# Performance work log

Hardware: AMD Instinct MI355X
Metric: run time of the kernel (lower is better)

The kernel has to match this reference:

```python
import jax, jax.numpy as jnp
import numpy as np

B, H, T, D = 2, 16, 2048, 64


def setup_inputs() -> dict:
    key = jax.random.key(0)
    kq, kk, kv = jax.random.split(key, 3)
    Q = jax.random.normal(kq, (B, H, T, D), dtype=jnp.float32)
    K = jax.random.normal(kk, (B, H, T, D), dtype=jnp.float32)
    V = jax.random.normal(kv, (B, H, T, D), dtype=jnp.float32)
    return {"Q": Q, "K": K, "V": V}


def reference(Q, K, V):
    # Q,K,V: [B,H,T,D]; causal self-attention with 1/sqrt(D) temperature.
    Bq, Hq, Tq, Dq = Q.shape
    temperature = jnp.asarray(Dq, Q.dtype) ** 0.5
    # [B,H,T,T] attention scores
    scores = jnp.einsum('bhqd,bhkd->bhqk', Q, K) / temperature
    causal = jnp.tril(jnp.ones((Tq, Tq), dtype=bool))  # [T,T]
    scores = jnp.where(causal[None, None, :, :], scores, jnp.finfo(Q.dtype).min)
    weights = jax.nn.softmax(scores, axis=-1)
    return jnp.einsum('bhqk,bhkd->bhqd', weights, V)
```

## Files before the change

### kernel.cpp

```cpp
#include <hip/hip_runtime.h>
#include <hip/hip_bf16.h>
#include <math.h>


#define BATCH 2
#define HEADS 16
#define SEQ   2048
#define DIM   64
#define QTILE 64
#define KTILE 64
#define NBH   (BATCH * HEADS)
#define NQT   (SEQ / QTILE)
#define NKT_G (SEQ / KTILE)
#define TILE_SHORTS 4096

typedef __attribute__((ext_vector_type(8))) short bf16x8;
typedef __attribute__((ext_vector_type(4))) short s16x4;
typedef __attribute__((ext_vector_type(2))) unsigned u32x2;
typedef __attribute__((ext_vector_type(4))) float f32x4;

__device__ inline short f2bf(float f) {
    unsigned u = __builtin_bit_cast(unsigned, f);
    u += 0x7fff + ((u >> 16) & 1);
    return (short)(u >> 16);
}

__device__ inline unsigned cvtpk(float a, float b) {
    unsigned r;
    asm("v_cvt_pk_bf16_f32 %0, %1, %2" : "=v"(r) : "v"(a), "v"(b));
    return r;
}

__device__ inline void gload16(const void* g, void* l) {
    __builtin_amdgcn_global_load_lds(
        (const __attribute__((address_space(1))) unsigned*)g,
        (__attribute__((address_space(3))) unsigned*)l, 16, 0, 0);
}

__global__ __launch_bounds__(256)
void prep_kv(const float* __restrict__ K, const float* __restrict__ V,
             short* __restrict__ Kswz, short* __restrict__ Vtswz) {
    const int tile = blockIdx.x;
    const int tid  = threadIdx.x;
    const float* Ksrc = K + (size_t)tile * TILE_SHORTS;
    const float* Vsrc = V + (size_t)tile * TILE_SHORTS;
    char* Kdst = (char*)(Kswz  + (size_t)tile * TILE_SHORTS);
    char* Vdst = (char*)(Vtswz + (size_t)tile * TILE_SHORTS);

    __shared__ float vt[64][65];

    const int r  = tid >> 2;
    const int c0 = (tid & 3) * 16;

    {
        short kh[16];
        #pragma unroll
        for (int j = 0; j < 16; j += 4) {
            const f32x4 v = *reinterpret_cast<const f32x4*>(Ksrc + (size_t)r * 64 + c0 + j);
            kh[j] = f2bf(v[0]); kh[j+1] = f2bf(v[1]); kh[j+2] = f2bf(v[2]); kh[j+3] = f2bf(v[3]);
        }
        const unsigned swz  = ((unsigned)r & 7) << 4;
        const unsigned base = (unsigned)r * 128 + (unsigned)c0 * 2;
        *reinterpret_cast<bf16x8*>(Kdst + (base ^ swz))        = *reinterpret_cast<bf16x8*>(&kh[0]);
        *reinterpret_cast<bf16x8*>(Kdst + ((base + 16) ^ swz)) = *reinterpret_cast<bf16x8*>(&kh[8]);
    }

    #pragma unroll
    for (int j = 0; j < 16; j += 4) {
        const f32x4 v = *reinterpret_cast<const f32x4*>(Vsrc + (size_t)r * 64 + c0 + j);
        vt[r][c0+j] = v[0]; vt[r][c0+j+1] = v[1]; vt[r][c0+j+2] = v[2]; vt[r][c0+j+3] = v[3];
    }
    __syncthreads();
    {
        const int d  = tid >> 2;
        const int k0 = (tid & 3) * 16;
        short vh[16];
        #pragma unroll
        for (int j = 0; j < 16; ++j) vh[j] = f2bf(vt[k0 + j][d]);
        const unsigned swz  = ((unsigned)d & 7) << 4;
        const unsigned base = (unsigned)d * 128 + (unsigned)k0 * 2;
        *reinterpret_cast<bf16x8*>(Vdst + (base ^ swz))        = *reinterpret_cast<bf16x8*>(&vh[0]);
        *reinterpret_cast<bf16x8*>(Vdst + ((base + 16) ^ swz)) = *reinterpret_cast<bf16x8*>(&vh[8]);
    }
}

__global__ __launch_bounds__(256, 4)
void fa_fwd(const float* __restrict__ Q, const short* __restrict__ Kswz,
            const short* __restrict__ Vtswz, float* __restrict__ O) {
    const int tid  = threadIdx.x;
    const int lane = tid & 63;
    const int wid  = tid >> 6;
    const int lo   = lane & 15;
    const int hi   = lane >> 4;

    const int idx = blockIdx.x;
    const int j   = idx >> 5;
    const int bh  = idx & 31;
    const int qt  = (j < 16) ? (31 - j) : (j - 16);
    const int q0  = qt * QTILE;

    const float* Qb = Q + (size_t)bh * SEQ * DIM;
    float*       Ob = O + (size_t)bh * SEQ * DIM;
    const size_t tbase = (size_t)bh * NKT_G * TILE_SHORTS;

    __shared__ short Klds[2][TILE_SHORTS];
    __shared__ short Vlds[2][TILE_SHORTS];
    __shared__ char  Plds[4][2048];

    const int nkt = qt + 1;

    auto stage = [&](int bb, int kt) {
        const short* Kt = Kswz  + tbase + (size_t)kt * TILE_SHORTS;
        const short* Vt = Vtswz + tbase + (size_t)kt * TILE_SHORTS;
        const int off = wid * 512 + lane * 8;
        gload16(Kt + off,        &Klds[bb][wid * 512]);
        gload16(Kt + 2048 + off, &Klds[bb][2048 + wid * 512]);
        gload16(Vt + off,        &Vlds[bb][wid * 512]);
        gload16(Vt + 2048 + off, &Vlds[bb][2048 + wid * 512]);
    };

    stage(0, 0);

    const unsigned swz = ((unsigned)(lo & 7)) << 4;
    const unsigned inner0 = ((unsigned)(lo * 128 + 0 * 64 + hi * 16)) ^ swz;
    const unsigned inner1 = ((unsigned)(lo * 128 + 1 * 64 + hi * 16)) ^ swz;
    const unsigned pbase = (unsigned)wid * 2048;
    unsigned pwr[4];
    #pragma unroll
    for (int t = 0; t < 4; ++t)
        pwr[t] = pbase + (((unsigned)(lo * 128 + t * 32 + hi * 8)) ^ swz);
    const unsigned prd0 = pbase + inner0;
    const unsigned prd1 = pbase + inner1;
    char* const P0 = (char*)Plds;

    const float SCL = 0.18033688011112042f;
    bf16x8 qf[2];
    {
        const int qrow = q0 + wid * 16 + lo;
        #pragma unroll
        for (int ks = 0; ks < 2; ++ks) {
            const float* src = Qb + (size_t)qrow * DIM + ks * 32 + hi * 8;
            const f32x4 a = *reinterpret_cast<const f32x4*>(src);
            const f32x4 b = *reinterpret_cast<const f32x4*>(src + 4);
            bf16x8 q;
            #pragma unroll
            for (int jj = 0; jj < 4; ++jj) {
                q[jj]     = f2bf(a[jj] * SCL);
                q[4 + jj] = f2bf(b[jj] * SCL);
            }
            qf[ks] = q;
        }
    }

    f32x4 oacc[4] = {};
    float rsum = 0.f;
    const int qg = q0 + wid * 16 + lo;

    __syncthreads();

    for (int kt = 0; kt < nkt; ++kt) {
        const int bb = kt & 1;
        if (kt + 1 < nkt) stage(bb ^ 1, kt + 1);

        const char* Kb = (const char*)Klds[bb];
        const char* Vb = (const char*)Vlds[bb];

        f32x4 st[4];
        __builtin_amdgcn_s_setprio(1);
        #pragma unroll
        for (int t = 0; t < 4; ++t) {
            const bf16x8 kf0 = *reinterpret_cast<const bf16x8*>(Kb + inner0 + t * 2048);
            const bf16x8 kf1 = *reinterpret_cast<const bf16x8*>(Kb + inner1 + t * 2048);
            f32x4 acc = {};
            acc = __builtin_amdgcn_mfma_f32_16x16x32_bf16(kf0, qf[0], acc, 0, 0, 0);
            acc = __builtin_amdgcn_mfma_f32_16x16x32_bf16(kf1, qf[1], acc, 0, 0, 0);
            st[t] = acc;
        }
        __builtin_amdgcn_s_setprio(0);

        const bool domask = (kt == nkt - 1);
        {
            float racc0 = 0.f, racc1 = 0.f;
            #pragma unroll
            for (int t = 0; t < 4; ++t) {
                float p[4];
                #pragma unroll
                for (int r = 0; r < 4; ++r) {
                    float arg = st[t][r];
                    if (domask) {
                        const int kg = kt * KTILE + t * 16 + hi * 4 + r;
                        if (kg > qg) arg = -1e30f;
                    }
                    p[r] = __builtin_amdgcn_exp2f(arg);
                }
                racc0 += p[0] + p[1];
                racc1 += p[2] + p[3];
                const u32x2 w = { cvtpk(p[0], p[1]), cvtpk(p[2], p[3]) };
                *reinterpret_cast<s16x4*>(P0 + pwr[t]) = __builtin_bit_cast(s16x4, w);
            }
            rsum += racc0 + racc1;
        }
        asm volatile("" ::: "memory");

        __builtin_amdgcn_s_setprio(1);
        {
            const bf16x8 pa0 = *reinterpret_cast<const bf16x8*>(P0 + prd0);
            const bf16x8 pa1 = *reinterpret_cast<const bf16x8*>(P0 + prd1);
            #pragma unroll
            for (int t = 0; t < 4; ++t) {
                const bf16x8 vf0 = *reinterpret_cast<const bf16x8*>(Vb + inner0 + t * 2048);
                const bf16x8 vf1 = *reinterpret_cast<const bf16x8*>(Vb + inner1 + t * 2048);
                oacc[t] = __builtin_amdgcn_mfma_f32_16x16x32_bf16(pa0, vf0, oacc[t], 0, 0, 0);
                oacc[t] = __builtin_amdgcn_mfma_f32_16x16x32_bf16(pa1, vf1, oacc[t], 0, 0, 0);
            }
        }
        __builtin_amdgcn_s_setprio(0);

        __syncthreads();
    }

    {
        float rs = rsum;
        rs += __shfl_xor(rs, 16, 64);
        rs += __shfl_xor(rs, 32, 64);
        const float vinv = 1.0f / rs;
        #pragma unroll
        for (int r = 0; r < 4; ++r) {
            const float inv_r = __shfl(vinv, hi * 4 + r, 64);
            const int q_idx = q0 + wid * 16 + hi * 4 + r;
            #pragma unroll
            for (int t = 0; t < 4; ++t)
                Ob[(size_t)q_idx * DIM + t * 16 + lo] = oacc[t][r] * inv_r;
        }
    }
}

extern "C" void kernel_launch(void* const* d_in, const int* in_sizes, int n_in,
                              void* d_out, int out_size, void* d_ws, size_t ws_size,
                              hipStream_t stream) {
    const float* Q = (const float*)d_in[0];
    const float* K = (const float*)d_in[1];
    const float* V = (const float*)d_in[2];
    float*       O = (float*)d_out;

    short* Kswz  = (short*)d_ws;
    short* Vtswz = (short*)d_ws + (size_t)NBH * NKT_G * TILE_SHORTS;

    prep_kv<<<dim3(NBH * NKT_G), dim3(256), 0, stream>>>(K, V, Kswz, Vtswz);
    fa_fwd<<<dim3(NBH * NQT), dim3(256), 0, stream>>>(Q, Kswz, Vtswz, O);
}
```

Before: 46.64 us.

## Load V fragments directly from global in MFMA register layout, drop V LDS staging

The prep kernel now writes V as a pre-fragmented image in which each lane's bf16x8 MFMA operand is contiguous, so each wave can load its V fragments straight from global memory into registers instead of staging them through double-buffered LDS. This removes the V LDS buffers and LDS reads and halves the async LDS copies per tile. The launch-bounds occupancy hint is also dropped. In exchange, every wave redundantly reads the full V tile from global/L2 each iteration, and those loads are not prefetched a tile ahead, so their latency may be exposed.

```diff
diff --git a/kernel.cpp b/kernel.cpp
--- a/kernel.cpp
+++ b/kernel.cpp
@@ -39,13 +39,13 @@
 
 __global__ __launch_bounds__(256)
 void prep_kv(const float* __restrict__ K, const float* __restrict__ V,
-             short* __restrict__ Kswz, short* __restrict__ Vtswz) {
+             short* __restrict__ Kswz, short* __restrict__ Vimg) {
     const int tile = blockIdx.x;
     const int tid  = threadIdx.x;
     const float* Ksrc = K + (size_t)tile * TILE_SHORTS;
     const float* Vsrc = V + (size_t)tile * TILE_SHORTS;
-    char* Kdst = (char*)(Kswz  + (size_t)tile * TILE_SHORTS);
-    char* Vdst = (char*)(Vtswz + (size_t)tile * TILE_SHORTS);
+    char* Kdst = (char*)(Kswz + (size_t)tile * TILE_SHORTS);
+    char* Vdst = (char*)(Vimg + (size_t)tile * TILE_SHORTS);
 
     __shared__ float vt[64][65];
 
@@ -71,22 +71,26 @@
         vt[r][c0+j] = v[0]; vt[r][c0+j+1] = v[1]; vt[r][c0+j+2] = v[2]; vt[r][c0+j+3] = v[3];
     }
     __syncthreads();
-    {
-        const int d  = tid >> 2;
-        const int k0 = (tid & 3) * 16;
-        short vh[16];
-        #pragma unroll
-        for (int j = 0; j < 16; ++j) vh[j] = f2bf(vt[k0 + j][d]);
-        const unsigned swz  = ((unsigned)d & 7) << 4;
-        const unsigned base = (unsigned)d * 128 + (unsigned)k0 * 2;
-        *reinterpret_cast<bf16x8*>(Vdst + (base ^ swz))        = *reinterpret_cast<bf16x8*>(&vh[0]);
-        *reinterpret_cast<bf16x8*>(Vdst + ((base + 16) ^ swz)) = *reinterpret_cast<bf16x8*>(&vh[8]);
-    }
-}
-
-__global__ __launch_bounds__(256, 4)
+
+    #pragma unroll
+    for (int s2 = 0; s2 < 2; ++s2) {
+        const int slot = tid + s2 * 256;
+        const int fi = slot >> 6;
+        const int l  = slot & 63;
+        const int t  = fi & 3;
+        const int ks = fi >> 2;
+        const int d  = t * 16 + (l & 15);
+        const int k0 = ks * 32 + (l >> 4) * 8;
+        short h[8];
+        #pragma unroll
+        for (int j = 0; j < 8; ++j) h[j] = f2bf(vt[k0 + j][d]);
+        *reinterpret_cast<bf16x8*>(Vdst + slot * 16) = *reinterpret_cast<bf16x8*>(h);
+    }
+}
+
+__global__ __launch_bounds__(256)
 void fa_fwd(const float* __restrict__ Q, const short* __restrict__ Kswz,
-            const short* __restrict__ Vtswz, float* __restrict__ O) {
+            const short* __restrict__ Vimg, float* __restrict__ O) {
     const int tid  = threadIdx.x;
     const int lane = tid & 63;
     const int wid  = tid >> 6;
@@ -104,19 +108,15 @@
     const size_t tbase = (size_t)bh * NKT_G * TILE_SHORTS;
 
     __shared__ short Klds[2][TILE_SHORTS];
-    __shared__ short Vlds[2][TILE_SHORTS];
     __shared__ char  Plds[4][2048];
 
     const int nkt = qt + 1;
 
     auto stage = [&](int bb, int kt) {
-        const short* Kt = Kswz  + tbase + (size_t)kt * TILE_SHORTS;
-        const short* Vt = Vtswz + tbase + (size_t)kt * TILE_SHORTS;
+        const short* Kt = Kswz + tbase + (size_t)kt * TILE_SHORTS;
         const int off = wid * 512 + lane * 8;
         gload16(Kt + off,        &Klds[bb][wid * 512]);
         gload16(Kt + 2048 + off, &Klds[bb][2048 + wid * 512]);
-        gload16(Vt + off,        &Vlds[bb][wid * 512]);
-        gload16(Vt + 2048 + off, &Vlds[bb][2048 + wid * 512]);
     };
 
     stage(0, 0);
@@ -155,6 +155,7 @@
     f32x4 oacc[4] = {};
     float rsum = 0.f;
     const int qg = q0 + wid * 16 + lo;
+    const unsigned lb = (unsigned)lane * 16;
 
     __syncthreads();
 
@@ -162,8 +163,16 @@
         const int bb = kt & 1;
         if (kt + 1 < nkt) stage(bb ^ 1, kt + 1);
 
+        const char* Vt = (const char*)(Vimg + tbase + (size_t)kt * TILE_SHORTS);
+        bf16x8 vf[2][4];
+        #pragma unroll
+        for (int ks = 0; ks < 2; ++ks)
+            #pragma unroll
+            for (int t = 0; t < 4; ++t)
+                vf[ks][t] = *reinterpret_cast<const bf16x8*>(
+                    Vt + (ks * 4 + t) * 1024 + lb);
+
         const char* Kb = (const char*)Klds[bb];
-        const char* Vb = (const char*)Vlds[bb];
 
         f32x4 st[4];
         __builtin_amdgcn_s_setprio(1);
@@ -208,10 +217,8 @@
             const bf16x8 pa1 = *reinterpret_cast<const bf16x8*>(P0 + prd1);
             #pragma unroll
             for (int t = 0; t < 4; ++t) {
-                const bf16x8 vf0 = *reinterpret_cast<const bf16x8*>(Vb + inner0 + t * 2048);
-                const bf16x8 vf1 = *reinterpret_cast<const bf16x8*>(Vb + inner1 + t * 2048);
-                oacc[t] = __builtin_amdgcn_mfma_f32_16x16x32_bf16(pa0, vf0, oacc[t], 0, 0, 0);
-                oacc[t] = __builtin_amdgcn_mfma_f32_16x16x32_bf16(pa1, vf1, oacc[t], 0, 0, 0);
+                oacc[t] = __builtin_amdgcn_mfma_f32_16x16x32_bf16(pa0, vf[0][t], oacc[t], 0, 0, 0);
+                oacc[t] = __builtin_amdgcn_mfma_f32_16x16x32_bf16(pa1, vf[1][t], oacc[t], 0, 0, 0);
             }
         }
         __builtin_amdgcn_s_setprio(0);
@@ -243,9 +250,9 @@
     const float* V = (const float*)d_in[2];
     float*       O = (float*)d_out;
 
-    short* Kswz  = (short*)d_ws;
-    short* Vtswz = (short*)d_ws + (size_t)NBH * NKT_G * TILE_SHORTS;
-
-    prep_kv<<<dim3(NBH * NKT_G), dim3(256), 0, stream>>>(K, V, Kswz, Vtswz);
-    fa_fwd<<<dim3(NBH * NQT), dim3(256), 0, stream>>>(Q, Kswz, Vtswz, O);
-}
+    short* Kswz = (short*)d_ws;
+    short* Vimg = (short*)d_ws + (size_t)NBH * NKT_G * TILE_SHORTS;
+
+    prep_kv<<<dim3(NBH * NKT_G), dim3(256), 0, stream>>>(K, V, Kswz, Vimg);
+    fa_fwd<<<dim3(NBH * NQT), dim3(256), 0, stream>>>(Q, Kswz, Vimg, O);
+}
```

Result: slower. 49.46 us (+6.0%).
